# Kernel tuning notes

Hardware: AMD Instinct MI355X
Metric: run time of the kernel (lower is better)

## Reference

```python
import jax, jax.numpy as jnp
import numpy as np

B, V, CODE_NUM = 64, 100, 4096
CODE_SIZE, ATT, VISIT, TIME, HID, OUT = 256, 128, 256, 64, 512, 90
TYPE_NUM = 32
NEG = -2.0 ** 31


def setup_inputs() -> dict:
    key = jax.random.key(0)
    ks = jax.random.split(key, 24)
    s = 0.02
    return {
        'code_x': jax.random.randint(ks[0], (B, V, CODE_NUM), 0, 2).astype(jnp.float32),
        'code_type0': jax.random.randint(ks[1], (CODE_NUM + 1,), 0, TYPE_NUM),
        'code_type1': jax.random.randint(ks[2], (CODE_NUM + 1,), 0, TYPE_NUM),
        'code_type2': jax.random.randint(ks[3], (CODE_NUM + 1,), 0, TYPE_NUM),
        'lens': jax.random.randint(ks[4], (B,), 1, V + 1),
        'intervals': jax.random.uniform(ks[5], (B, V), dtype=jnp.float32),
        # encoder: code + 3 type embedding tables (rows 1..code_num used)
        'code_emb': jax.random.normal(ks[6], (CODE_NUM + 1, CODE_SIZE), jnp.float32) * s,
        't0_emb': jax.random.normal(ks[7], (TYPE_NUM, CODE_SIZE), jnp.float32) * s,
        't1_emb': jax.random.normal(ks[8], (TYPE_NUM, CODE_SIZE), jnp.float32) * s,
        't2_emb': jax.random.normal(ks[9], (TYPE_NUM, CODE_SIZE), jnp.float32) * s,
        # visit self-attention (no bias, per nn.Linear(..., bias=False))
        'Wq': jax.random.normal(ks[10], (CODE_SIZE, ATT), jnp.float32) * s,
        'Wk': jax.random.normal(ks[11], (CODE_SIZE, ATT), jnp.float32) * s,
        'Wv': jax.random.normal(ks[12], (CODE_SIZE, VISIT), jnp.float32) * s,
        # time embedding Linear(1, time_size)
        'time_w': jax.random.normal(ks[13], (TIME,), jnp.float32) * s,
        'time_b': jnp.zeros((TIME,), jnp.float32),
        # GRUCell params (torch layout: gates ordered r,z,n)
        'gru_Wih': jax.random.normal(ks[14], (3 * HID, VISIT + TIME), jnp.float32) * s,
        'gru_Whh': jax.random.normal(ks[15], (3 * HID, HID), jnp.float32) * s,
        'gru_bih': jnp.zeros((3 * HID,), jnp.float32),
        'gru_bhh': jnp.zeros((3 * HID,), jnp.float32),
        # classifier
        'cls_W': jax.random.normal(ks[16], (OUT, HID), jnp.float32) * s,
        'cls_b': jnp.zeros((OUT,), jnp.float32),
    }


def reference(code_x, code_type0, code_type1, code_type2, lens, intervals,
              code_emb, t0_emb, t1_emb, t2_emb, Wq, Wk, Wv, time_w, time_b,
              gru_Wih, gru_Whh, gru_bih, gru_bhh, cls_W, cls_b):
    # --- Encoder (vectorized): multi-hot slot i corresponds to code id i+1 ---
    E = (code_emb[1:]
         + t0_emb[code_type0[1:]]
         + t1_emb[code_type1[1:]]
         + t2_emb[code_type2[1:]])                      # [CODE_NUM, CODE_SIZE]
    active = (code_x > 0).astype(E.dtype)               # [B, V, CODE_NUM]
    counts = jnp.maximum(active.sum(-1, keepdims=True), 1.0)
    v_emb_ini = jnp.einsum('bvc,cd->bvd', active, E) / counts  # mean over codes
    visit_mask = jnp.arange(V)[None, :] < lens[:, None]        # [B, V]
    v_emb_ini = v_emb_ini * visit_mask[..., None]              # padded visits stay 0

    # --- Context-aware visit self-attention ---
    Q = v_emb_ini @ Wq                                   # [B, V, ATT]
    K = v_emb_ini @ Wk
    Vv = v_emb_ini @ Wv                                  # [B, V, VISIT]
    alpha = jnp.einsum('bqa,bka->bqk', Q, K)
    alpha = jnp.where(visit_mask[:, None, :], alpha, NEG)  # mask keys
    alpha = jax.nn.softmax(alpha, axis=2)
    v_emb = jnp.einsum('bqk,bkd->bqd', alpha, Vv) + Vv     # [B, V, VISIT]

    # --- Time-aware input ---
    t_emb = intervals[..., None] * time_w + time_b         # [B, V, TIME]
    x = jnp.concatenate([v_emb, t_emb], axis=-1)           # [B, V, VISIT+TIME]

    # --- GRU over visits, gated by per-patient length ---
    def step(h, xm):
        xt, mt = xm                                        # xt [B,D], mt [B]
        gi = xt @ gru_Wih.T + gru_bih
        gh = h @ gru_Whh.T + gru_bhh
        ir, iz, inn = jnp.split(gi, 3, axis=-1)
        hr, hz, hn = jnp.split(gh, 3, axis=-1)
        r = jax.nn.sigmoid(ir + hr)
        z = jax.nn.sigmoid(iz + hz)
        n = jnp.tanh(inn + r * hn)
        h_new = (1.0 - z) * n + z * h
        h = jnp.where(mt[:, None], h_new, h)
        return h, None

    h0 = jnp.zeros((B, HID), x.dtype)
    h_final, _ = jax.lax.scan(step, h0, (x.transpose(1, 0, 2), visit_mask.T))

    # --- Classifier (dropout p=0 -> identity) ---
    return jax.nn.sigmoid(h_final @ cls_W.T + cls_b)       # [B, OUT]
```

## Files before the change

### kernel.cpp

```cpp
#include <hip/hip_runtime.h>
#include <hip/hip_bf16.h>

typedef float  f32x4 __attribute__((ext_vector_type(4)));
typedef short  s16x8 __attribute__((ext_vector_type(8)));
typedef short  s16x4 __attribute__((ext_vector_type(4)));

#define NEGBIG -1e30f

__device__ __forceinline__ unsigned short f2b(float f) {
    union { float f; unsigned u; } c; c.f = f;
    unsigned r = c.u + 0x7FFF + ((c.u >> 16) & 1);
    return (unsigned short)(r >> 16);
}
__device__ __forceinline__ float b2f(unsigned short h) {
    union { unsigned u; float f; } c; c.u = ((unsigned)h) << 16;
    return c.f;
}
__device__ __forceinline__ float sigm(float x) { return 1.f / (1.f + __expf(-x)); }

__device__ __forceinline__ s16x8 ld_b128_sc(const unsigned short* p) {
    s16x8 r;
    asm volatile("global_load_dwordx4 %0, %1, off sc0 sc1" : "=v"(r) : "v"(p));
    return r;
}
__device__ __forceinline__ void st_b64_sc(unsigned short* p, unsigned int x, unsigned int y) {
    union { unsigned int u[2]; unsigned long long ull; } v; v.u[0] = x; v.u[1] = y;
    asm volatile("global_store_dwordx2 %0, %1, off sc0 sc1" :: "v"(p), "v"(v.ull) : "memory");
}
__device__ __forceinline__ void st_b128f_sc(float* p, f32x4 v) {
    asm volatile("global_store_dwordx4 %0, %1, off sc0 sc1" :: "v"(p), "v"(v) : "memory");
}

__global__ __launch_bounds__(256) void prep_all(const float* code_emb, const int* ct0, const int* ct1, const int* ct2,
                                                const float* t0e, const float* t1e, const float* t2e,
                                                const float* Wq, const float* Wk, const float* Wv,
                                                const float* gWih, const float* gWhh,
                                                unsigned short* ET, unsigned short* wcat,
                                                unsigned short* wih, unsigned short* whh,
                                                int* flags, unsigned short* hb0) {
    __shared__ float tile[64][65];
    const int bid = blockIdx.x;
    const int t = threadIdx.x;
    if (bid < 256) {
        const int d0 = (bid & 3) * 64, c0 = (bid >> 2) * 64;
        for (int p = 0; p < 16; ++p) {
            int idx = p * 256 + t;
            int dl = idx & 63, cl = idx >> 6;
            int code = c0 + cl + 1;
            int d = d0 + dl;
            float v = code_emb[code * 256 + d] + t0e[ct0[code] * 256 + d]
                    + t1e[ct1[code] * 256 + d] + t2e[ct2[code] * 256 + d];
            tile[dl][cl] = v;
        }
        __syncthreads();
        for (int p = 0; p < 2; ++p) {
            int idx = p * 256 + t;
            int dl = idx >> 3, ch = idx & 7;
            s16x8 pk;
#pragma unroll
            for (int e = 0; e < 8; ++e) pk[e] = (short)f2b(tile[dl][ch * 8 + e]);
            *(s16x8*)(ET + (size_t)(d0 + dl) * 4096 + c0 + ch * 8) = pk;
        }
    } else {
        if (bid >= 504) {
            int idx = (bid - 504) * 256 + t;
            for (int i = idx; i < 1024; i += 2048) flags[i] = 0;
            for (int i = idx; i < 32768; i += 2048) hb0[i] = 0;
        }
        int idx = (bid - 256) * 256 + t;
        const int stride = 256 * 256;
        const int N1 = 131072, N2 = 491520, N3 = 786432;
        for (; idx < N1 + N2 + N3; idx += stride) {
            if (idx < N1) {
                int n = idx >> 8, k = idx & 255;
                float v;
                if (n < 128) v = Wq[k * 128 + n];
                else if (n < 256) v = Wk[k * 128 + (n - 128)];
                else v = Wv[k * 256 + (n - 256)];
                wcat[n * 256 + k] = f2b(v);
            } else if (idx < N1 + N2) {
                int i = idx - N1; wih[i] = f2b(gWih[i]);
            } else {
                int i = idx - N1 - N2; whh[i] = f2b(gWhh[i]);
            }
        }
    }
}

__global__ __launch_bounds__(256) void enc_gemm(const float* code_x, const unsigned short* ET,
                                                const int* lens, unsigned short* Vb) {
    __shared__ __align__(16) char sm[4096 + 32768 + 128];
    char* As = sm;
    char* Bs = sm + 4096;
    float* cl = (float*)(sm + 4096 + 32768);
    const int m0 = blockIdx.x * 32;
    const int t = threadIdx.x, l = t & 63, w = t >> 6;
    const int lr = l & 15, lq = l >> 4, l7 = l & 7;
    const int sr = t >> 3, sc = t & 7;
    const int bn = t >> 3, bc = t & 7;
    const float* gabase = code_x + (size_t)(m0 + sr) * 4096 + sc * 8;
    f32x4 acc[2][4];
#pragma unroll
    for (int a = 0; a < 2; ++a)
#pragma unroll
        for (int b = 0; b < 4; ++b) acc[a][b] = (f32x4){0.f, 0.f, 0.f, 0.f};
    int cnt = 0;

    f32x4 a0A, a1A, a0B, a1B;
    s16x8 bA[8], bB[8];

#define ENC_ISSUE(SLOT, IT) do {                                                     \
    const int k0_ = (IT) * 64;                                                       \
    a0##SLOT = *(const f32x4*)(gabase + k0_);                                        \
    a1##SLOT = *(const f32x4*)(gabase + k0_ + 4);                                    \
    _Pragma("unroll")                                                                \
    for (int rd_ = 0; rd_ < 8; ++rd_)                                                \
        b##SLOT[rd_] = *(const s16x8*)(ET + (size_t)(rd_ * 32 + bn) * 4096 + k0_ + bc * 8); \
} while (0)

#define ENC_CONSUME(SLOT, NEXTIT) do {                                               \
    s16x8 ap_;                                                                       \
    _Pragma("unroll")                                                                \
    for (int e_ = 0; e_ < 4; ++e_) { bool on_ = a0##SLOT[e_] > 0.f; ap_[e_] = on_ ? (short)0x3F80 : (short)0; cnt += on_ ? 1 : 0; } \
    _Pragma("unroll")                                                                \
    for (int e_ = 0; e_ < 4; ++e_) { bool on_ = a1##SLOT[e_] > 0.f; ap_[4 + e_] = on_ ? (short)0x3F80 : (short)0; cnt += on_ ? 1 : 0; } \
    *(s16x8*)(As + sr * 128 + ((sc ^ (sr & 7)) << 4)) = ap_;                         \
    _Pragma("unroll")                                                                \
    for (int rd_ = 0; rd_ < 8; ++rd_) {                                              \
        int n_ = rd_ * 32 + bn;                                                      \
        *(s16x8*)(Bs + n_ * 128 + ((bc ^ (n_ & 7)) << 4)) = b##SLOT[rd_];            \
    }                                                                                \
    if ((NEXTIT) < 64) ENC_ISSUE(SLOT, NEXTIT);                                      \
    __syncthreads();                                                                 \
    _Pragma("unroll")                                                                \
    for (int kk_ = 0; kk_ < 2; ++kk_) {                                              \
        const int cp_ = kk_ * 4 + lq;                                                \
        s16x8 af_[2], bf_[4];                                                        \
        _Pragma("unroll")                                                            \
        for (int mt_ = 0; mt_ < 2; ++mt_)                                            \
            af_[mt_] = *(const s16x8*)(As + (mt_ * 16 + lr) * 128 + ((cp_ ^ l7) << 4)); \
        _Pragma("unroll")                                                            \
        for (int nt_ = 0; nt_ < 4; ++nt_)                                            \
            bf_[nt_] = *(const s16x8*)(Bs + ((w * 4 + nt_) * 16 + lr) * 128 + ((cp_ ^ l7) << 4)); \
        _Pragma("unroll")                                                            \
        for (int mt_ = 0; mt_ < 2; ++mt_)                                            \
            _Pragma("unroll")                                                        \
            for (int nt_ = 0; nt_ < 4; ++nt_)                                        \
                acc[mt_][nt_] = __builtin_amdgcn_mfma_f32_16x16x32_bf16(af_[mt_], bf_[nt_], acc[mt_][nt_], 0, 0, 0); \
    }                                                                                \
    __syncthreads();                                                                 \
} while (0)

    ENC_ISSUE(A, 0);
    ENC_ISSUE(B, 1);
    for (int base = 0; base < 64; base += 2) {
        ENC_CONSUME(A, base + 2);
        ENC_CONSUME(B, base + 3);
    }
#undef ENC_ISSUE
#undef ENC_CONSUME

    float fc = (float)cnt;
    fc += __shfl_xor(fc, 1); fc += __shfl_xor(fc, 2); fc += __shfl_xor(fc, 4);
    if (sc == 0) cl[sr] = fmaxf(fc, 1.f);
    __syncthreads();
#pragma unroll
    for (int mt = 0; mt < 2; ++mt)
#pragma unroll
        for (int i = 0; i < 4; ++i) {
            int m = mt * 16 + lq * 4 + i;
            int gm = m0 + m;
            float rc = 1.f / cl[m];
            unsigned bi = (unsigned)gm / 100u;
            unsigned vi = (unsigned)gm - bi * 100u;
            float msk = ((int)vi < lens[bi]) ? 1.f : 0.f;
#pragma unroll
            for (int nt = 0; nt < 4; ++nt) {
                int n = (w * 4 + nt) * 16 + lr;
                Vb[(size_t)gm * 256 + n] = f2b(acc[mt][nt][i] * rc * msk);
            }
        }
}

__global__ __launch_bounds__(256) void gemm_bf16(const unsigned short* A, const unsigned short* Bm,
                                                 int K, int Ntot, int mode,
                                                 unsigned short* outp, const float* bias) {
    __shared__ __align__(16) char sm[4096 + 32768];
    char* As = sm;
    char* Bs = sm + 4096;
    const int m0 = blockIdx.x * 32;
    const int n0 = blockIdx.y * 256;
    const int t = threadIdx.x, l = t & 63, w = t >> 6;
    const int lr = l & 15, lq = l >> 4, l7 = l & 7;
    const int sr = t >> 3, sc = t & 7;
    const int bn = t >> 3, bc = t & 7;
    const int iters = K >> 6;
    f32x4 acc[2][4];
#pragma unroll
    for (int a = 0; a < 2; ++a)
#pragma unroll
        for (int b = 0; b < 4; ++b) acc[a][b] = (f32x4){0.f, 0.f, 0.f, 0.f};

    s16x8 avA, avB;
    s16x8 bA[8], bB[8];

#define GB_ISSUE(SLOT, IT) do {                                                      \
    const int k0_ = (IT) * 64;                                                       \
    av##SLOT = *(const s16x8*)(A + (size_t)(m0 + sr) * K + k0_ + sc * 8);            \
    _Pragma("unroll")                                                                \
    for (int rd_ = 0; rd_ < 8; ++rd_)                                                \
        b##SLOT[rd_] = *(const s16x8*)(Bm + (size_t)(n0 + rd_ * 32 + bn) * K + k0_ + bc * 8); \
} while (0)

#define GB_CONSUME(SLOT, NEXTIT) do {                                                \
    *(s16x8*)(As + sr * 128 + ((sc ^ (sr & 7)) << 4)) = av##SLOT;                    \
    _Pragma("unroll")                                                                \
    for (int rd_ = 0; rd_ < 8; ++rd_) {                                              \
        int n_ = rd_ * 32 + bn;                                                      \
        *(s16x8*)(Bs + n_ * 128 + ((bc ^ (n_ & 7)) << 4)) = b##SLOT[rd_];            \
    }                                                                                \
    if ((NEXTIT) < iters) GB_ISSUE(SLOT, NEXTIT);                                    \
    __syncthreads();                                                                 \
    _Pragma("unroll")                                                                \
    for (int kk_ = 0; kk_ < 2; ++kk_) {                                              \
        const int cp_ = kk_ * 4 + lq;                                                \
        s16x8 af_[2], bf_[4];                                                        \
        _Pragma("unroll")                                                            \
        for (int mt_ = 0; mt_ < 2; ++mt_)                                            \
            af_[mt_] = *(const s16x8*)(As + (mt_ * 16 + lr) * 128 + ((cp_ ^ l7) << 4)); \
        _Pragma("unroll")                                                            \
        for (int nt_ = 0; nt_ < 4; ++nt_)                                            \
            bf_[nt_] = *(const s16x8*)(Bs + ((w * 4 + nt_) * 16 + lr) * 128 + ((cp_ ^ l7) << 4)); \
        _Pragma("unroll")                                                            \
        for (int mt_ = 0; mt_ < 2; ++mt_)                                            \
            _Pragma("unroll")                                                        \
            for (int nt_ = 0; nt_ < 4; ++nt_)                                        \
                acc[mt_][nt_] = __builtin_amdgcn_mfma_f32_16x16x32_bf16(af_[mt_], bf_[nt_], acc[mt_][nt_], 0, 0, 0); \
    }                                                                                \
    __syncthreads();                                                                 \
} while (0)

    GB_ISSUE(A, 0);
    if (iters > 1) GB_ISSUE(B, 1);
    for (int base = 0; base < iters; base += 2) {
        GB_CONSUME(A, base + 2);
        if (base + 1 < iters) GB_CONSUME(B, base + 3);
    }
#undef GB_ISSUE
#undef GB_CONSUME

#pragma unroll
    for (int mt = 0; mt < 2; ++mt)
#pragma unroll
        for (int i = 0; i < 4; ++i) {
            int gm = m0 + mt * 16 + lq * 4 + i;
#pragma unroll
            for (int nt = 0; nt < 4; ++nt) {
                int n = n0 + (w * 4 + nt) * 16 + lr;
                float v = acc[mt][nt][i];
                if (mode == 1) v += bias[n];
                outp[(size_t)gm * Ntot + n] = f2b(v);
            }
        }
}

__global__ __launch_bounds__(256) void attn_kernel(const unsigned short* QKV, const int* lens,
                                                   const float* intervals, const float* time_w, const float* time_b,
                                                   unsigned short* X) {
    __shared__ __align__(16) char sm[28672 + 32768];
    char* Pb = sm;
    char* VTb = sm + 28672;
    const int b = blockIdx.x;
    const int h = blockIdx.y;
    const int t = threadIdx.x, l = t & 63, w = t >> 6;
    const int lr = l & 15, lq = l >> 4;
    const int lenb = lens[b];
    for (int p = 0; p < 7; ++p) {
        int idx = p * 256 + t;
        *(f32x4*)(Pb + idx * 16) = (f32x4){0.f, 0.f, 0.f, 0.f};
    }
    __syncthreads();
    f32x4 S[2][7];
#pragma unroll
    for (int a = 0; a < 2; ++a)
#pragma unroll
        for (int c = 0; c < 7; ++c) S[a][c] = (f32x4){0.f, 0.f, 0.f, 0.f};
#pragma unroll
    for (int kk = 0; kk < 4; ++kk) {
        s16x8 qa[2], kb[7];
#pragma unroll
        for (int mi = 0; mi < 2; ++mi) {
            int mt = 2 * w + mi;
            if (mt > 6) continue;
            int row = b * 100 + mt * 16 + lr;
            qa[mi] = *(const s16x8*)(QKV + (size_t)row * 512 + kk * 32 + lq * 8);
        }
#pragma unroll
        for (int nt = 0; nt < 7; ++nt) {
            int row = b * 100 + nt * 16 + lr;
            kb[nt] = *(const s16x8*)(QKV + (size_t)row * 512 + 128 + kk * 32 + lq * 8);
        }
#pragma unroll
        for (int mi = 0; mi < 2; ++mi) {
            int mt = 2 * w + mi;
            if (mt > 6) continue;
#pragma unroll
            for (int nt = 0; nt < 7; ++nt)
                S[mi][nt] = __builtin_amdgcn_mfma_f32_16x16x32_bf16(qa[mi], kb[nt], S[mi][nt], 0, 0, 0);
        }
    }
#pragma unroll
    for (int mi = 0; mi < 2; ++mi) {
        int mt = 2 * w + mi;
        if (mt > 6) continue;
        float sv[7][4];
#pragma unroll
        for (int nt = 0; nt < 7; ++nt) {
            int j = nt * 16 + lr;
#pragma unroll
            for (int i = 0; i < 4; ++i)
                sv[nt][i] = (j < lenb) ? S[mi][nt][i] : NEGBIG;
        }
#pragma unroll
        for (int i = 0; i < 4; ++i) {
            float mx = sv[0][i];
#pragma unroll
            for (int nt = 1; nt < 7; ++nt) mx = fmaxf(mx, sv[nt][i]);
            mx = fmaxf(mx, __shfl_xor(mx, 1));
            mx = fmaxf(mx, __shfl_xor(mx, 2));
            mx = fmaxf(mx, __shfl_xor(mx, 4));
            mx = fmaxf(mx, __shfl_xor(mx, 8));
            float e[7], sum = 0.f;
#pragma unroll
            for (int nt = 0; nt < 7; ++nt) { e[nt] = __expf(sv[nt][i] - mx); sum += e[nt]; }
            sum += __shfl_xor(sum, 1);
            sum += __shfl_xor(sum, 2);
            sum += __shfl_xor(sum, 4);
            sum += __shfl_xor(sum, 8);
            float rs = 1.f / sum;
            int m = mt * 16 + lq * 4 + i;
#pragma unroll
            for (int nt = 0; nt < 7; ++nt) {
                int j = nt * 16 + lr;
                *(unsigned short*)(Pb + m * 256 + (((j >> 3) ^ (m & 7)) << 4) + ((j & 7) << 1)) = f2b(e[nt] * rs);
            }
        }
    }
    __syncthreads();
    for (int p = 0; p < 8; ++p) {
        int idx = p * 256 + t;
        *(f32x4*)(VTb + idx * 16) = (f32x4){0.f, 0.f, 0.f, 0.f};
    }
    __syncthreads();
    for (int p = 0; p < 7; ++p) {
        int ci = p * 256 + t;
        if (ci < 1600) {
            int j = ci >> 4, d8 = ci & 15;
            s16x8 vv = *(const s16x8*)(QKV + (size_t)(b * 100 + j) * 512 + 256 + h * 128 + d8 * 8);
#pragma unroll
            for (int e = 0; e < 8; ++e) {
                int dl = d8 * 8 + e;
                *(unsigned short*)(VTb + dl * 256 + (((j >> 3) ^ (dl & 7)) << 4) + ((j & 7) << 1)) = (unsigned short)vv[e];
            }
        }
    }
    __syncthreads();
    f32x4 O[2][8];
#pragma unroll
    for (int a = 0; a < 2; ++a)
#pragma unroll
        for (int c = 0; c < 8; ++c) O[a][c] = (f32x4){0.f, 0.f, 0.f, 0.f};
#pragma unroll
    for (int kk = 0; kk < 4; ++kk) {
        s16x8 pa[2];
#pragma unroll
        for (int mi = 0; mi < 2; ++mi) {
            int mt = 2 * w + mi;
            if (mt > 6) continue;
            int m = mt * 16 + lr;
            pa[mi] = *(const s16x8*)(Pb + m * 256 + (((kk * 4 + lq) ^ (m & 7)) << 4));
        }
#pragma unroll
        for (int nt = 0; nt < 8; ++nt) {
            int dl = nt * 16 + lr;
            s16x8 vb = *(const s16x8*)(VTb + dl * 256 + (((kk * 4 + lq) ^ (dl & 7)) << 4));
#pragma unroll
            for (int mi = 0; mi < 2; ++mi) {
                int mt = 2 * w + mi;
                if (mt > 6) continue;
                O[mi][nt] = __builtin_amdgcn_mfma_f32_16x16x32_bf16(pa[mi], vb, O[mi][nt], 0, 0, 0);
            }
        }
    }
#pragma unroll
    for (int mi = 0; mi < 2; ++mi) {
        int mt = 2 * w + mi;
        if (mt > 6) continue;
#pragma unroll
        for (int i = 0; i < 4; ++i) {
            int m = mt * 16 + lq * 4 + i;
            if (m < 100) {
#pragma unroll
                for (int nt = 0; nt < 8; ++nt) {
                    int dl = nt * 16 + lr;
                    float res = b2f(*(unsigned short*)(VTb + dl * 256 + (((m >> 3) ^ (dl & 7)) << 4) + ((m & 7) << 1)));
                    X[(size_t)(b * 100 + m) * 320 + h * 128 + dl] = f2b(O[mi][nt][i] + res);
                }
            }
        }
    }
    if (h == 0) {
        for (int p = 0; p < 25; ++p) {
            int idx = p * 256 + t;
            int m = idx >> 6, d = idx & 63;
            float val = intervals[b * 100 + m] * time_w[d] + time_b[d];
            X[(size_t)(b * 100 + m) * 320 + 256 + d] = f2b(val);
        }
    }
}

__global__ __launch_bounds__(256, 1) void gru_kernel(const unsigned short* GIb, const unsigned short* WHH,
                                                     const float* gbhh, const int* lens,
                                                     unsigned short* hb0, unsigned short* hb1, float* hf,
                                                     int* flags, const float* clsW, const float* clsb, float* out) {
    const int bid = blockIdx.x;
    const int t = threadIdx.x, l = t & 63, w = t >> 6;
    const int lo = l & 15, hi = l >> 4;
    const int d0 = bid * 16;
    const int batch = w * 16 + lo;
    const int j0 = d0 + hi * 4;
    int ml;
    {
        int v = lens[l];
        v = max(v, __shfl_xor(v, 1));  v = max(v, __shfl_xor(v, 2));
        v = max(v, __shfl_xor(v, 4));  v = max(v, __shfl_xor(v, 8));
        v = max(v, __shfl_xor(v, 16)); v = max(v, __shfl_xor(v, 32));
        ml = v;
    }
    const int len = lens[batch];
    const f32x4 bhr4 = *(const f32x4*)(gbhh + j0);
    const f32x4 bhz4 = *(const f32x4*)(gbhh + 512 + j0);
    const f32x4 bhn4 = *(const f32x4*)(gbhh + 1024 + j0);
    s16x8 Wf[3][16];
#pragma unroll
    for (int g = 0; g < 3; ++g)
#pragma unroll
        for (int kk = 0; kk < 16; ++kk)
            Wf[g][kk] = *(const s16x8*)(WHH + (size_t)(g * 512 + d0 + lo) * 512 + kk * 32 + hi * 8);
    float ho[4] = {0.f, 0.f, 0.f, 0.f};
    const size_t hrow = (size_t)batch * 512 + j0;
    const size_t arow = (size_t)batch * 512 + hi * 8;
    const size_t gi_row = (size_t)batch * 100;

    s16x4 pgr = *(const s16x4*)(GIb + gi_row * 1536 + j0);
    s16x4 pgz = *(const s16x4*)(GIb + gi_row * 1536 + 512 + j0);
    s16x4 pgn = *(const s16x4*)(GIb + gi_row * 1536 + 1024 + j0);

    for (int step = 0; step < ml; ++step) {
        const unsigned short* hb = (step & 1) ? hb1 : hb0;
        unsigned short* hn = (step & 1) ? hb0 : hb1;
        s16x8 af[16];
#pragma unroll
        for (int kk = 0; kk < 16; ++kk)
            af[kk] = ld_b128_sc(hb + arow + kk * 32);
        asm volatile("s_waitcnt vmcnt(0)" ::: "memory");
        __builtin_amdgcn_sched_barrier(0);
        f32x4 ar = (f32x4){0.f,0.f,0.f,0.f}, az = ar, an = ar;
#pragma unroll
        for (int kk = 0; kk < 16; ++kk) {
            ar = __builtin_amdgcn_mfma_f32_16x16x32_bf16(Wf[0][kk], af[kk], ar, 0, 0, 0);
            az = __builtin_amdgcn_mfma_f32_16x16x32_bf16(Wf[1][kk], af[kk], az, 0, 0, 0);
            an = __builtin_amdgcn_mfma_f32_16x16x32_bf16(Wf[2][kk], af[kk], an, 0, 0, 0);
        }
        {
            float hv4[4];
#pragma unroll
            for (int i = 0; i < 4; ++i) {
                float r = sigm(b2f((unsigned short)pgr[i]) + ar[i] + bhr4[i]);
                float z = sigm(b2f((unsigned short)pgz[i]) + az[i] + bhz4[i]);
                float n = tanhf(b2f((unsigned short)pgn[i]) + r * (an[i] + bhn4[i]));
                float hv = (step < len) ? ((1.f - z) * n + z * ho[i]) : ho[i];
                ho[i] = hv; hv4[i] = hv;
            }
            unsigned px = (unsigned)f2b(hv4[0]) | ((unsigned)f2b(hv4[1]) << 16);
            unsigned py = (unsigned)f2b(hv4[2]) | ((unsigned)f2b(hv4[3]) << 16);
            st_b64_sc(hn + hrow, px, py);
        }
        asm volatile("s_waitcnt vmcnt(0)" ::: "memory");
        __syncthreads();
        if (t == 0)
            __hip_atomic_store(flags + bid * 16, step + 1, __ATOMIC_RELAXED, __HIP_MEMORY_SCOPE_AGENT);
        if (step + 1 < ml) {
            pgr = *(const s16x4*)(GIb + (gi_row + step + 1) * 1536 + j0);
            pgz = *(const s16x4*)(GIb + (gi_row + step + 1) * 1536 + 512 + j0);
            pgn = *(const s16x4*)(GIb + (gi_row + step + 1) * 1536 + 1024 + j0);
        }
        if (w == 0) {
            int guard = 0;
            while (true) {
                int v = (l < 32) ? __hip_atomic_load(flags + l * 16, __ATOMIC_RELAXED, __HIP_MEMORY_SCOPE_AGENT) : (step + 1);
                if (__all(v >= step + 1)) break;
                if (++guard > (1 << 20)) break;
                __builtin_amdgcn_s_sleep(1);
            }
        }
        __syncthreads();
    }
    {
        f32x4 hv = (f32x4){ho[0], ho[1], ho[2], ho[3]};
        st_b128f_sc(hf + (size_t)batch * 512 + j0, hv);
    }
    asm volatile("s_waitcnt vmcnt(0)" ::: "memory");
    __syncthreads();
    if (t == 0)
        __hip_atomic_store(flags + bid * 16, ml + 1, __ATOMIC_RELAXED, __HIP_MEMORY_SCOPE_AGENT);
    if (w == 0) {
        int guard = 0;
        while (true) {
            int v = (l < 32) ? __hip_atomic_load(flags + l * 16, __ATOMIC_RELAXED, __HIP_MEMORY_SCOPE_AGENT) : (ml + 1);
            if (__all(v >= ml + 1)) break;
            if (++guard > (1 << 20)) break;
            __builtin_amdgcn_s_sleep(1);
        }
    }
    __syncthreads();
    if (bid < 30) {
        int bb = t >> 2, qq = t & 3;
        int c0 = bid * 3;
        float s0 = 0.f, s1 = 0.f, s2 = 0.f;
        for (int kc = 0; kc < 32; ++kc) {
            int k = qq * 128 + kc * 4;
            f32x4 hv = *(const f32x4*)(hf + bb * 512 + k);
            f32x4 w0 = *(const f32x4*)(clsW + (c0 + 0) * 512 + k);
            f32x4 w1 = *(const f32x4*)(clsW + (c0 + 1) * 512 + k);
            f32x4 w2 = *(const f32x4*)(clsW + (c0 + 2) * 512 + k);
            s0 += hv[0] * w0[0] + hv[1] * w0[1] + hv[2] * w0[2] + hv[3] * w0[3];
            s1 += hv[0] * w1[0] + hv[1] * w1[1] + hv[2] * w1[2] + hv[3] * w1[3];
            s2 += hv[0] * w2[0] + hv[1] * w2[1] + hv[2] * w2[2] + hv[3] * w2[3];
        }
        s0 += __shfl_xor(s0, 1); s0 += __shfl_xor(s0, 2);
        s1 += __shfl_xor(s1, 1); s1 += __shfl_xor(s1, 2);
        s2 += __shfl_xor(s2, 1); s2 += __shfl_xor(s2, 2);
        if (qq == 0) {
            out[bb * 90 + c0 + 0] = sigm(s0 + clsb[c0 + 0]);
            out[bb * 90 + c0 + 1] = sigm(s1 + clsb[c0 + 1]);
            out[bb * 90 + c0 + 2] = sigm(s2 + clsb[c0 + 2]);
        }
    }
}

extern "C" void kernel_launch(void* const* d_in, const int* in_sizes, int n_in,
                              void* d_out, int out_size, void* d_ws, size_t ws_size,
                              hipStream_t stream) {
    const float* code_x   = (const float*)d_in[0];
    const int*   ct0      = (const int*)d_in[1];
    const int*   ct1      = (const int*)d_in[2];
    const int*   ct2      = (const int*)d_in[3];
    const int*   lens     = (const int*)d_in[4];
    const float* intervals= (const float*)d_in[5];
    const float* code_emb = (const float*)d_in[6];
    const float* t0e      = (const float*)d_in[7];
    const float* t1e      = (const float*)d_in[8];
    const float* t2e      = (const float*)d_in[9];
    const float* Wq       = (const float*)d_in[10];
    const float* Wk       = (const float*)d_in[11];
    const float* Wv       = (const float*)d_in[12];
    const float* time_w   = (const float*)d_in[13];
    const float* time_b   = (const float*)d_in[14];
    const float* gWih     = (const float*)d_in[15];
    const float* gWhh     = (const float*)d_in[16];
    const float* gbih     = (const float*)d_in[17];
    const float* gbhh     = (const float*)d_in[18];
    const float* clsW     = (const float*)d_in[19];
    const float* clsb     = (const float*)d_in[20];

    char* ws = (char*)d_ws;
    const size_t ET_OFF   = 0;
    const size_t WCAT_OFF = 2097152;
    const size_t WIH_OFF  = 2359296;
    const size_t WHH_OFF  = 3342336;
    const size_t V_OFF    = 4915200;
    const size_t QKV_OFF  = 8192000;
    const size_t X_OFF    = 14778368;
    const size_t GI_OFF   = 18874368;
    const size_t HB0_OFF  = 38535168;
    const size_t HB1_OFF  = 38600704;
    const size_t HF_OFF   = 38666240;
    const size_t FLG_OFF  = 38797312;

    unsigned short* ET   = (unsigned short*)(ws + ET_OFF);
    unsigned short* WCAT = (unsigned short*)(ws + WCAT_OFF);
    unsigned short* WIH  = (unsigned short*)(ws + WIH_OFF);
    unsigned short* WHH  = (unsigned short*)(ws + WHH_OFF);
    unsigned short* Vb   = (unsigned short*)(ws + V_OFF);
    unsigned short* QKV  = (unsigned short*)(ws + QKV_OFF);
    unsigned short* Xb   = (unsigned short*)(ws + X_OFF);
    unsigned short* GIb  = (unsigned short*)(ws + GI_OFF);
    unsigned short* hb0  = (unsigned short*)(ws + HB0_OFF);
    unsigned short* hb1  = (unsigned short*)(ws + HB1_OFF);
    float*          hf   = (float*)(ws + HF_OFF);
    int*            flags= (int*)(ws + FLG_OFF);

    prep_all<<<512, 256, 0, stream>>>(code_emb, ct0, ct1, ct2, t0e, t1e, t2e,
                                      Wq, Wk, Wv, gWih, gWhh,
                                      ET, WCAT, WIH, WHH, flags, hb0);
    enc_gemm<<<200, 256, 0, stream>>>(code_x, ET, lens, Vb);
    gemm_bf16<<<dim3(200, 2), 256, 0, stream>>>(Vb, WCAT, 256, 512, 2, QKV, nullptr);
    attn_kernel<<<dim3(64, 2), 256, 0, stream>>>(QKV, lens, intervals, time_w, time_b, Xb);
    gemm_bf16<<<dim3(200, 6), 256, 0, stream>>>(Xb, WIH, 320, 1536, 1, GIb, gbih);
    gru_kernel<<<32, 256, 0, stream>>>(GIb, WHH, gbhh, lens, hb0, hb1, hf, flags, clsW, clsb, (float*)d_out);
}
```

Measured before the change: 734.1 us.

## Halve GRU persistent blocks, each handling 32 hidden units per step

The persistent GRU kernel now runs on 16 blocks instead of 32. Each block computes two 16-column tiles of the hidden state, keeping twice as many recurrent weight fragments in registers. The per-step inter-block flag barrier polls 16 flags instead of 32, which cuts the cost of cross-block synchronisation on the sequential critical path. The trade-offs are double the MFMA work per step per block and much higher register pressure (96 s16x8 weight fragments), which could cause spills. The classifier loop is adjusted so the 16 blocks still cover all 90 outputs.

```diff
diff --git a/kernel.cpp b/kernel.cpp
--- a/kernel.cpp
+++ b/kernel.cpp
@@ -426,9 +426,8 @@
     const int bid = blockIdx.x;
     const int t = threadIdx.x, l = t & 63, w = t >> 6;
     const int lo = l & 15, hi = l >> 4;
-    const int d0 = bid * 16;
+    const int d0 = bid * 32;
     const int batch = w * 16 + lo;
-    const int j0 = d0 + hi * 4;
     int ml;
     {
         int v = lens[l];
@@ -438,23 +437,34 @@
         ml = v;
     }
     const int len = lens[batch];
-    const f32x4 bhr4 = *(const f32x4*)(gbhh + j0);
-    const f32x4 bhz4 = *(const f32x4*)(gbhh + 512 + j0);
-    const f32x4 bhn4 = *(const f32x4*)(gbhh + 1024 + j0);
-    s16x8 Wf[3][16];
+    int j0t[2];
+    f32x4 bhr4[2], bhz4[2], bhn4[2];
+#pragma unroll
+    for (int jt = 0; jt < 2; ++jt) {
+        j0t[jt] = d0 + jt * 16 + hi * 4;
+        bhr4[jt] = *(const f32x4*)(gbhh + j0t[jt]);
+        bhz4[jt] = *(const f32x4*)(gbhh + 512 + j0t[jt]);
+        bhn4[jt] = *(const f32x4*)(gbhh + 1024 + j0t[jt]);
+    }
+    s16x8 Wf[3][2][16];
 #pragma unroll
     for (int g = 0; g < 3; ++g)
 #pragma unroll
-        for (int kk = 0; kk < 16; ++kk)
-            Wf[g][kk] = *(const s16x8*)(WHH + (size_t)(g * 512 + d0 + lo) * 512 + kk * 32 + hi * 8);
-    float ho[4] = {0.f, 0.f, 0.f, 0.f};
-    const size_t hrow = (size_t)batch * 512 + j0;
+        for (int jt = 0; jt < 2; ++jt)
+#pragma unroll
+            for (int kk = 0; kk < 16; ++kk)
+                Wf[g][jt][kk] = *(const s16x8*)(WHH + (size_t)(g * 512 + d0 + jt * 16 + lo) * 512 + kk * 32 + hi * 8);
+    float ho[2][4] = {{0.f,0.f,0.f,0.f},{0.f,0.f,0.f,0.f}};
     const size_t arow = (size_t)batch * 512 + hi * 8;
     const size_t gi_row = (size_t)batch * 100;
 
-    s16x4 pgr = *(const s16x4*)(GIb + gi_row * 1536 + j0);
-    s16x4 pgz = *(const s16x4*)(GIb + gi_row * 1536 + 512 + j0);
-    s16x4 pgn = *(const s16x4*)(GIb + gi_row * 1536 + 1024 + j0);
+    s16x4 pgr[2], pgz[2], pgn[2];
+#pragma unroll
+    for (int jt = 0; jt < 2; ++jt) {
+        pgr[jt] = *(const s16x4*)(GIb + gi_row * 1536 + j0t[jt]);
+        pgz[jt] = *(const s16x4*)(GIb + gi_row * 1536 + 512 + j0t[jt]);
+        pgn[jt] = *(const s16x4*)(GIb + gi_row * 1536 + 1024 + j0t[jt]);
+    }
 
     for (int step = 0; step < ml; ++step) {
         const unsigned short* hb = (step & 1) ? hb1 : hb0;
@@ -465,40 +475,49 @@
             af[kk] = ld_b128_sc(hb + arow + kk * 32);
         asm volatile("s_waitcnt vmcnt(0)" ::: "memory");
         __builtin_amdgcn_sched_barrier(0);
-        f32x4 ar = (f32x4){0.f,0.f,0.f,0.f}, az = ar, an = ar;
+        f32x4 ar[2], az[2], an[2];
+#pragma unroll
+        for (int jt = 0; jt < 2; ++jt) { ar[jt] = (f32x4){0.f,0.f,0.f,0.f}; az[jt] = ar[jt]; an[jt] = ar[jt]; }
 #pragma unroll
         for (int kk = 0; kk < 16; ++kk) {
-            ar = __builtin_amdgcn_mfma_f32_16x16x32_bf16(Wf[0][kk], af[kk], ar, 0, 0, 0);
-            az = __builtin_amdgcn_mfma_f32_16x16x32_bf16(Wf[1][kk], af[kk], az, 0, 0, 0);
-            an = __builtin_amdgcn_mfma_f32_16x16x32_bf16(Wf[2][kk], af[kk], an, 0, 0, 0);
-        }
-        {
+#pragma unroll
+            for (int jt = 0; jt < 2; ++jt) {
+                ar[jt] = __builtin_amdgcn_mfma_f32_16x16x32_bf16(Wf[0][jt][kk], af[kk], ar[jt], 0, 0, 0);
+                az[jt] = __builtin_amdgcn_mfma_f32_16x16x32_bf16(Wf[1][jt][kk], af[kk], az[jt], 0, 0, 0);
+                an[jt] = __builtin_amdgcn_mfma_f32_16x16x32_bf16(Wf[2][jt][kk], af[kk], an[jt], 0, 0, 0);
+            }
+        }
+#pragma unroll
+        for (int jt = 0; jt < 2; ++jt) {
             float hv4[4];
 #pragma unroll
             for (int i = 0; i < 4; ++i) {
-                float r = sigm(b2f((unsigned short)pgr[i]) + ar[i] + bhr4[i]);
-                float z = sigm(b2f((unsigned short)pgz[i]) + az[i] + bhz4[i]);
-                float n = tanhf(b2f((unsigned short)pgn[i]) + r * (an[i] + bhn4[i]));
-                float hv = (step < len) ? ((1.f - z) * n + z * ho[i]) : ho[i];
-                ho[i] = hv; hv4[i] = hv;
+                float r = sigm(b2f((unsigned short)pgr[jt][i]) + ar[jt][i] + bhr4[jt][i]);
+                float z = sigm(b2f((unsigned short)pgz[jt][i]) + az[jt][i] + bhz4[jt][i]);
+                float n = tanhf(b2f((unsigned short)pgn[jt][i]) + r * (an[jt][i] + bhn4[jt][i]));
+                float hv = (step < len) ? ((1.f - z) * n + z * ho[jt][i]) : ho[jt][i];
+                ho[jt][i] = hv; hv4[i] = hv;
             }
             unsigned px = (unsigned)f2b(hv4[0]) | ((unsigned)f2b(hv4[1]) << 16);
             unsigned py = (unsigned)f2b(hv4[2]) | ((unsigned)f2b(hv4[3]) << 16);
-            st_b64_sc(hn + hrow, px, py);
+            st_b64_sc(hn + (size_t)batch * 512 + j0t[jt], px, py);
         }
         asm volatile("s_waitcnt vmcnt(0)" ::: "memory");
         __syncthreads();
         if (t == 0)
             __hip_atomic_store(flags + bid * 16, step + 1, __ATOMIC_RELAXED, __HIP_MEMORY_SCOPE_AGENT);
         if (step + 1 < ml) {
-            pgr = *(const s16x4*)(GIb + (gi_row + step + 1) * 1536 + j0);
-            pgz = *(const s16x4*)(GIb + (gi_row + step + 1) * 1536 + 512 + j0);
-            pgn = *(const s16x4*)(GIb + (gi_row + step + 1) * 1536 + 1024 + j0);
+#pragma unroll
+            for (int jt = 0; jt < 2; ++jt) {
+                pgr[jt] = *(const s16x4*)(GIb + (gi_row + step + 1) * 1536 + j0t[jt]);
+                pgz[jt] = *(const s16x4*)(GIb + (gi_row + step + 1) * 1536 + 512 + j0t[jt]);
+                pgn[jt] = *(const s16x4*)(GIb + (gi_row + step + 1) * 1536 + 1024 + j0t[jt]);
+            }
         }
         if (w == 0) {
             int guard = 0;
             while (true) {
-                int v = (l < 32) ? __hip_atomic_load(flags + l * 16, __ATOMIC_RELAXED, __HIP_MEMORY_SCOPE_AGENT) : (step + 1);
+                int v = (l < 16) ? __hip_atomic_load(flags + l * 16, __ATOMIC_RELAXED, __HIP_MEMORY_SCOPE_AGENT) : (step + 1);
                 if (__all(v >= step + 1)) break;
                 if (++guard > (1 << 20)) break;
                 __builtin_amdgcn_s_sleep(1);
@@ -506,9 +525,10 @@
         }
         __syncthreads();
     }
-    {
-        f32x4 hv = (f32x4){ho[0], ho[1], ho[2], ho[3]};
-        st_b128f_sc(hf + (size_t)batch * 512 + j0, hv);
+#pragma unroll
+    for (int jt = 0; jt < 2; ++jt) {
+        f32x4 hv = (f32x4){ho[jt][0], ho[jt][1], ho[jt][2], ho[jt][3]};
+        st_b128f_sc(hf + (size_t)batch * 512 + j0t[jt], hv);
     }
     asm volatile("s_waitcnt vmcnt(0)" ::: "memory");
     __syncthreads();
@@ -517,16 +537,15 @@
     if (w == 0) {
         int guard = 0;
         while (true) {
-            int v = (l < 32) ? __hip_atomic_load(flags + l * 16, __ATOMIC_RELAXED, __HIP_MEMORY_SCOPE_AGENT) : (ml + 1);
+            int v = (l < 16) ? __hip_atomic_load(flags + l * 16, __ATOMIC_RELAXED, __HIP_MEMORY_SCOPE_AGENT) : (ml + 1);
             if (__all(v >= ml + 1)) break;
             if (++guard > (1 << 20)) break;
             __builtin_amdgcn_s_sleep(1);
         }
     }
     __syncthreads();
-    if (bid < 30) {
+    for (int c0 = bid * 3; c0 < 90; c0 += 48) {
         int bb = t >> 2, qq = t & 3;
-        int c0 = bid * 3;
         float s0 = 0.f, s1 = 0.f, s2 = 0.f;
         for (int kc = 0; kc < 32; ++kc) {
             int k = qq * 128 + kc * 4;
@@ -608,5 +627,5 @@
     gemm_bf16<<<dim3(200, 2), 256, 0, stream>>>(Vb, WCAT, 256, 512, 2, QKV, nullptr);
     attn_kernel<<<dim3(64, 2), 256, 0, stream>>>(QKV, lens, intervals, time_w, time_b, Xb);
     gemm_bf16<<<dim3(200, 6), 256, 0, stream>>>(Xb, WIH, 320, 1536, 1, GIb, gbih);
-    gru_kernel<<<32, 256, 0, stream>>>(GIb, WHH, gbhh, lens, hb0, hb1, hf, flags, clsW, clsb, (float*)d_out);
-}
+    gru_kernel<<<16, 256, 0, stream>>>(GIb, WHH, gbhh, lens, hb0, hb1, hf, flags, clsW, clsb, (float*)d_out);
+}
```

Result: slower. 1.062 ms (+44.7%).
